# Kernel tuning notes

Measured on AMD Instinct MI355X. Metric: run time of the kernel, lower is better.

## Reference

```python
import jax, jax.numpy as jnp
import numpy as np

# Dims: N parameter samples, M patches, C tracked compartments (S is implicit),
# TIMESTEPS sequential SIR-metapopulation steps.
N, M, C, TIMESTEPS = 256, 128, 3, 200


def setup_inputs() -> dict:
    key = jax.random.key(0)
    k1, k2, k3, k4 = jax.random.split(key, 4)
    R = jax.random.uniform(k1, (N, M, M), jnp.float32)          # mobility matrix (row-normalized in reference)
    T = jax.random.uniform(k2, (N, C, C), jnp.float32) * 0.3    # compartment transition matrix (scaled so rho stays in [0,1])
    rho0 = jax.random.uniform(k3, (N, M, C), jnp.float32) * 0.01  # small initial infected fractions
    beta = jax.random.uniform(k4, (N, 1), jnp.float32) * 0.5    # per-sample infection rate (infect_params)
    return {"R": R, "T": T, "rho0": rho0, "beta": beta}


def _infect_prob(prev_rho, R, pop, neff, beta):
    # Contact infection ('beta_contact'):
    #   ninf[n,k] = sum_j pop[j] * prev_rho[n,j,0] * R[n,j,k]
    # This equals summing neff_compartments[..., 0] over the source-patch axis,
    # without materializing the (N, M, M, C) tensor the TF code builds.
    ninf = jnp.einsum('j,nj,njk->nk', pop, prev_rho[..., 0], R)
    return beta * ninf / neff  # (N, M)


def reference(R, T, rho0, beta):
    R = R / jnp.sum(R, axis=-1, keepdims=True)
    pop = jnp.ones((M,), R.dtype)  # default populations
    # neff = populations @ R; constant across timesteps, hoisted out of the loop
    neff = jnp.einsum('j,njk->nk', pop, R)  # (N, M)
    e0 = jnp.zeros((C,), R.dtype).at[0].set(1.0)  # new infections enter compartment 0

    def step(prev_rho, _):
        p = _infect_prob(prev_rho, R, pop, neff, beta)                    # (N, M)
        new_inf = (1.0 - prev_rho.sum(-1)) * jnp.einsum('njk,nk->nj', R, p)  # S * (R @ p)
        rho = jnp.einsum('njk,nkl->njl', prev_rho, T) + new_inf[:, :, None] * e0
        rho = jnp.clip(rho, 0.0, 1.0)
        return rho, prev_rho  # write prev_rho at step i, then advance (matches TF body)

    _, trajs = jax.lax.scan(step, rho0, None, length=TIMESTEPS)  # (T, N, M, C)
    trajs = trajs.astype(jnp.float32)
    # AddSusceptibleLayer: prepend S = 1 - sum(compartments), transpose to (N, T, M, C+1)
    S = 1.0 - trajs.sum(-1)
    out = jnp.concatenate([S[..., None], trajs], axis=-1)
    return jnp.transpose(out, (1, 0, 2, 3))
```

## Files before the change

### kernel.cpp

```cpp
#include <hip/hip_runtime.h>

namespace {

constexpr int NS = 256;
constexpr int MP = 128;
constexpr int TSTEPS = 200;
constexpr int BLK = 512;

typedef _Float16 half8 __attribute__((ext_vector_type(8)));
typedef float f32x4 __attribute__((ext_vector_type(4)));

__device__ __forceinline__ float4 ldg4(const float* p) {
  return *reinterpret_cast<const float4*>(p);
}
__device__ __forceinline__ float clamp01(float v) {
  return fminf(fmaxf(v, 0.0f), 1.0f);
}
__device__ __forceinline__ void step_barrier() {
  asm volatile("s_waitcnt lgkmcnt(0)" ::: "memory");
  __builtin_amdgcn_s_barrier();
  asm volatile("" ::: "memory");
}
__device__ __forceinline__ float dot2(unsigned a, unsigned b, float c) {
  float d;
  asm("v_dot2_f32_f16 %0, %1, %2, %3" : "=v"(d) : "v"(a), "v"(b), "v"(c));
  return d;
}
__device__ __forceinline__ unsigned pkrtz(float a, float b) {
  typedef __fp16 h2v __attribute__((ext_vector_type(2)));
  h2v r = __builtin_amdgcn_cvt_pkrtz(a, b);
  return __builtin_bit_cast(unsigned, r);
}
__device__ __forceinline__ float dpp_xor1(float x) {
  int yi = __builtin_amdgcn_update_dpp(0, __float_as_int(x), 0xB1, 0xF, 0xF, true);
  return __int_as_float(yi);
}
__device__ __forceinline__ int qidx16(int row, int ch) {
  return (row << 4) + (ch ^ ((row >> 3) & 7));
}
__device__ __forceinline__ half8 h8(uint4 v) {
  return __builtin_bit_cast(half8, v);
}

__global__ __launch_bounds__(BLK, 2)
void sir_meta_kernel(const float* __restrict__ Rg,
                     const float* __restrict__ Tg,
                     const float* __restrict__ rho0g,
                     const float* __restrict__ betag,
                     float* __restrict__ outg)
{
  __shared__ __align__(16) float rs[MP];
  __shared__ __align__(16) float sbin[MP];
  __shared__ __align__(16) float scr[BLK];
  __shared__ __align__(16) unsigned xh[2][64];
  __shared__ __align__(16) uint4 q16[MP * 16];
  __shared__ __align__(16) uint4 gh[MP * 16];

  const int tid = threadIdx.x;
  const int n = blockIdx.x;
  const float* __restrict__ Rn = Rg + (size_t)n * MP * MP;

  {
    const int wave = tid >> 6;
    const int lane = tid & 63;
    const int half = lane >> 5;
    const int l32 = lane & 31;
    for (int it = 0; it < 8; ++it) {
      const int row = wave * 16 + it * 2 + half;
      float4 v = ldg4(Rn + row * MP + l32 * 4);
      float s = (v.x + v.y) + (v.z + v.w);
      s += __shfl_xor(s, 1);
      s += __shfl_xor(s, 2);
      s += __shfl_xor(s, 4);
      s += __shfl_xor(s, 8);
      s += __shfl_xor(s, 16);
      if (l32 == 0) rs[row] = 1.0f / s;
    }
  }
  __syncthreads();

  {
    const int c = tid & 127;
    const int h = tid >> 7;
    float a = 0.0f;
    #pragma unroll 8
    for (int i = 0; i < 32; ++i) {
      const int ig = h * 32 + i;
      a = fmaf(Rn[ig * MP + c], rs[ig], a);
    }
    scr[tid] = a;
  }
  __syncthreads();
  if (tid < 128)
    sbin[tid] = sqrtf(betag[n] /
        (((scr[tid] + scr[tid + 128]) + (scr[tid + 256] + scr[tid + 384]))));
  __syncthreads();

  {
    #pragma unroll
    for (int u = 0; u < 4; ++u) {
      const int fi8 = u * BLK + tid;
      const int r = fi8 >> 4, c8 = fi8 & 15;
      float4 lo = ldg4(Rn + r * MP + c8 * 8);
      float4 hi = ldg4(Rn + r * MP + c8 * 8 + 4);
      float4 s0 = *reinterpret_cast<const float4*>(&sbin[c8 * 8]);
      float4 s1 = *reinterpret_cast<const float4*>(&sbin[c8 * 8 + 4]);
      uint4 w;
      w.x = pkrtz(lo.x * s0.x, lo.y * s0.y);
      w.y = pkrtz(lo.z * s0.z, lo.w * s0.w);
      w.z = pkrtz(hi.x * s1.x, hi.y * s1.y);
      w.w = pkrtz(hi.z * s1.z, hi.w * s1.w);
      q16[qidx16(r, c8)] = w;
    }
  }
  __syncthreads();

  {
    const int wv = tid >> 6;
    const int g4 = (tid >> 4) & 3;
    const int k4 = tid & 15;
    const int rb = wv * 16 + g4 * 4;
    const int cb = k4 * 8;
    float acc[4][8];
    #pragma unroll
    for (int r = 0; r < 4; ++r)
      #pragma unroll
      for (int c = 0; c < 8; ++c) acc[r][c] = 0.0f;
    #pragma unroll 4
    for (int ch = 0; ch < 16; ++ch) {
      uint4 qa[4], qb[8];
      #pragma unroll
      for (int r = 0; r < 4; ++r) qa[r] = q16[qidx16(rb + r, ch)];
      #pragma unroll
      for (int c = 0; c < 8; ++c) qb[c] = q16[qidx16(cb + c, ch)];
      #pragma unroll
      for (int r = 0; r < 4; ++r) {
        #pragma unroll
        for (int c = 0; c < 8; ++c) {
          float a = acc[r][c];
          a = dot2(qa[r].x, qb[c].x, a);
          a = dot2(qa[r].y, qb[c].y, a);
          a = dot2(qa[r].z, qb[c].z, a);
          a = dot2(qa[r].w, qb[c].w, a);
          acc[r][c] = a;
        }
      }
    }
    float rsc[8];
    #pragma unroll
    for (int c = 0; c < 8; ++c) rsc[c] = rs[cb + c];
    #pragma unroll
    for (int r = 0; r < 4; ++r) {
      const float rr = rs[rb + r];
      uint4 w;
      w.x = pkrtz(acc[r][0] * rr * rsc[0], acc[r][1] * rr * rsc[1]);
      w.y = pkrtz(acc[r][2] * rr * rsc[2], acc[r][3] * rr * rsc[3]);
      w.z = pkrtz(acc[r][4] * rr * rsc[4], acc[r][5] * rr * rsc[5]);
      w.w = pkrtz(acc[r][6] * rr * rsc[6], acc[r][7] * rr * rsc[7]);
      gh[(rb + r) * 16 + k4] = w;
    }
  }
  __syncthreads();

  const int w = tid >> 6;
  const int l = tid & 63;
  const int col = l & 15;
  const int kg = l >> 4;
  const int jrow = 16 * w + 4 * kg + col;
  const bool writer = (col < 4);

  uint4 af0 = gh[(16 * w + col) * 16 + 0 + kg];
  uint4 af1 = gh[(16 * w + col) * 16 + 4 + kg];
  uint4 af2 = gh[(16 * w + col) * 16 + 8 + kg];
  uint4 af3 = gh[(16 * w + col) * 16 + 12 + kg];

  const float* Tn = Tg + n * 9;
  const float T00 = Tn[0], T01 = Tn[1], T02 = Tn[2];
  const float T10 = Tn[3], T11 = Tn[4], T12 = Tn[5];
  const float T20 = Tn[6], T21 = Tn[7], T22 = Tn[8];

  float r0 = 0.f, r1 = 0.f, r2 = 0.f;
  if (writer) {
    const float* rp = rho0g + ((size_t)n * MP + jrow) * 3;
    r0 = rp[0]; r1 = rp[1]; r2 = rp[2];
  }
  if (tid < 64) {
    const float* xp = rho0g + ((size_t)n * MP + 2 * tid) * 3;
    xh[0][tid] = pkrtz(xp[0], xp[3]);
  }
  __syncthreads();

  float4* outp = reinterpret_cast<float4*>(outg) + (size_t)n * TSTEPS * MP + jrow;
  const bool xwriter = writer && ((col & 1) == 0);
  const int xslot = jrow >> 1;

  for (int s = 0; s < TSTEPS; ++s) {
    const uint4* xq4 = reinterpret_cast<const uint4*>(&xh[s & 1][0]);
    const uint4 b0 = xq4[kg];
    const uint4 b1 = xq4[4 + kg];
    const uint4 b2 = xq4[8 + kg];
    const uint4 b3 = xq4[12 + kg];

    const float S = 1.0f - ((r0 + r1) + r2);
    if (writer) *outp = make_float4(S, r0, r1, r2);
    outp += MP;

    f32x4 accA = {0.f, 0.f, 0.f, 0.f};
    f32x4 accB = {0.f, 0.f, 0.f, 0.f};
    accA = __builtin_amdgcn_mfma_f32_16x16x32_f16(h8(af0), h8(b0), accA, 0, 0, 0);
    accB = __builtin_amdgcn_mfma_f32_16x16x32_f16(h8(af1), h8(b1), accB, 0, 0, 0);
    accA = __builtin_amdgcn_mfma_f32_16x16x32_f16(h8(af2), h8(b2), accA, 0, 0, 0);
    accB = __builtin_amdgcn_mfma_f32_16x16x32_f16(h8(af3), h8(b3), accB, 0, 0, 0);

    const float tA0 = (col & 1) ? accA[1] : accA[0];
    const float tA1 = (col & 1) ? accA[3] : accA[2];
    const float tB0 = (col & 1) ? accB[1] : accB[0];
    const float tB1 = (col & 1) ? accB[3] : accB[2];
    const float y = ((col & 2) ? tA1 : tA0) + ((col & 2) ? tB1 : tB0);

    const float ni = S * y;
    const float n0 = clamp01(fmaf(r0, T00, fmaf(r1, T10, fmaf(r2, T20, ni))));
    const float n1 = clamp01(fmaf(r0, T01, fmaf(r1, T11, r2 * T21)));
    const float n2 = clamp01(fmaf(r0, T02, fmaf(r1, T12, r2 * T22)));

    const float nb = dpp_xor1(n0);
    if (xwriter) xh[(s & 1) ^ 1][xslot] = pkrtz(n0, nb);

    r0 = n0; r1 = n1; r2 = n2;

    step_barrier();
  }
}

}

extern "C" void kernel_launch(void* const* d_in, const int* in_sizes, int n_in,
                              void* d_out, int out_size, void* d_ws, size_t ws_size,
                              hipStream_t stream)
{
  const float* Rg    = (const float*)d_in[0];
  const float* Tg    = (const float*)d_in[1];
  const float* rho0g = (const float*)d_in[2];
  const float* betag = (const float*)d_in[3];
  float* outg = (float*)d_out;
  sir_meta_kernel<<<NS, BLK, 0, stream>>>(Rg, Tg, rho0g, betag, outg);
}
```

Measured before the change: 74.07 us.

## Replicate full mat-vec in every wave to drop per-step block barriers

Each wave now holds all 8 row-blocks of the fp16 G matrix in registers and computes the full 128-row mat-vec itself every step. The next step's B operand is exchanged with ds_bpermute inside the wave instead of through double-buffered LDS. This removes the block-wide barrier from every timestep. In exchange each wave issues 8x more MFMAs per step, raises register pressure from holding 32 uint4 fragments, and has each lane track two rows.

```diff
diff --git a/kernel.cpp b/kernel.cpp
--- a/kernel.cpp
+++ b/kernel.cpp
@@ -16,11 +16,6 @@
 __device__ __forceinline__ float clamp01(float v) {
   return fminf(fmaxf(v, 0.0f), 1.0f);
 }
-__device__ __forceinline__ void step_barrier() {
-  asm volatile("s_waitcnt lgkmcnt(0)" ::: "memory");
-  __builtin_amdgcn_s_barrier();
-  asm volatile("" ::: "memory");
-}
 __device__ __forceinline__ float dot2(unsigned a, unsigned b, float c) {
   float d;
   asm("v_dot2_f32_f16 %0, %1, %2, %3" : "=v"(d) : "v"(a), "v"(b), "v"(c));
@@ -31,9 +26,8 @@
   h2v r = __builtin_amdgcn_cvt_pkrtz(a, b);
   return __builtin_bit_cast(unsigned, r);
 }
-__device__ __forceinline__ float dpp_xor1(float x) {
-  int yi = __builtin_amdgcn_update_dpp(0, __float_as_int(x), 0xB1, 0xF, 0xF, true);
-  return __int_as_float(yi);
+__device__ __forceinline__ unsigned bperm(int addr, unsigned src) {
+  return (unsigned)__builtin_amdgcn_ds_bpermute(addr, (int)src);
 }
 __device__ __forceinline__ int qidx16(int row, int ch) {
   return (row << 4) + (ch ^ ((row >> 3) & 7));
@@ -52,7 +46,7 @@
   __shared__ __align__(16) float rs[MP];
   __shared__ __align__(16) float sbin[MP];
   __shared__ __align__(16) float scr[BLK];
-  __shared__ __align__(16) unsigned xh[2][64];
+  __shared__ __align__(16) unsigned xh[64];
   __shared__ __align__(16) uint4 q16[MP * 16];
   __shared__ __align__(16) uint4 gh[MP * 16];
 
@@ -160,75 +154,117 @@
       gh[(rb + r) * 16 + k4] = w;
     }
   }
+  if (tid < 64) {
+    const float* xp = rho0g + ((size_t)n * MP + 2 * tid) * 3;
+    xh[tid] = pkrtz(xp[0], xp[3]);
+  }
   __syncthreads();
 
   const int w = tid >> 6;
   const int l = tid & 63;
   const int col = l & 15;
   const int kg = l >> 4;
-  const int jrow = 16 * w + 4 * kg + col;
-  const bool writer = (col < 4);
-
-  uint4 af0 = gh[(16 * w + col) * 16 + 0 + kg];
-  uint4 af1 = gh[(16 * w + col) * 16 + 4 + kg];
-  uint4 af2 = gh[(16 * w + col) * 16 + 8 + kg];
-  uint4 af3 = gh[(16 * w + col) * 16 + 12 + kg];
+  const bool t1 = (col & 1) != 0;
+  const bool i0 = (col & 2) != 0;
+  const bool i1 = (col & 4) != 0;
+  const bool i2 = (col & 8) != 0;
+  const int Istar = col >> 1;
+  const int rowA = 16 * Istar + 4 * kg + 2 * (col & 1);
+
+  uint4 af[8][4];
+  #pragma unroll
+  for (int I = 0; I < 8; ++I)
+    #pragma unroll
+    for (int c = 0; c < 4; ++c)
+      af[I][c] = gh[(16 * I + col) * 16 + 4 * c + kg];
+
+  int baddr[4][4];
+  #pragma unroll
+  for (int c = 0; c < 4; ++c)
+    #pragma unroll
+    for (int j = 0; j < 4; ++j) {
+      const int m = 16 * c + 4 * kg + j;
+      baddr[c][j] = 4 * (2 * (m >> 3) + (m & 1) + 16 * ((m >> 1) & 3));
+    }
+
+  const uint4* xq4 = reinterpret_cast<const uint4*>(xh);
+  uint4 bf0 = xq4[kg];
+  uint4 bf1 = xq4[4 + kg];
+  uint4 bf2 = xq4[8 + kg];
+  uint4 bf3 = xq4[12 + kg];
 
   const float* Tn = Tg + n * 9;
   const float T00 = Tn[0], T01 = Tn[1], T02 = Tn[2];
   const float T10 = Tn[3], T11 = Tn[4], T12 = Tn[5];
   const float T20 = Tn[6], T21 = Tn[7], T22 = Tn[8];
 
-  float r0 = 0.f, r1 = 0.f, r2 = 0.f;
-  if (writer) {
-    const float* rp = rho0g + ((size_t)n * MP + jrow) * 3;
-    r0 = rp[0]; r1 = rp[1]; r2 = rp[2];
-  }
-  if (tid < 64) {
-    const float* xp = rho0g + ((size_t)n * MP + 2 * tid) * 3;
-    xh[0][tid] = pkrtz(xp[0], xp[3]);
-  }
-  __syncthreads();
-
-  float4* outp = reinterpret_cast<float4*>(outg) + (size_t)n * TSTEPS * MP + jrow;
-  const bool xwriter = writer && ((col & 1) == 0);
-  const int xslot = jrow >> 1;
+  const float* rp = rho0g + ((size_t)n * MP + rowA) * 3;
+  float a0 = rp[0], a1 = rp[1], a2 = rp[2];
+  float b0 = rp[3], b1 = rp[4], b2 = rp[5];
+
+  const bool storer = (Istar == w);
+  float4* outp = reinterpret_cast<float4*>(outg) + (size_t)n * TSTEPS * MP + rowA;
 
   for (int s = 0; s < TSTEPS; ++s) {
-    const uint4* xq4 = reinterpret_cast<const uint4*>(&xh[s & 1][0]);
-    const uint4 b0 = xq4[kg];
-    const uint4 b1 = xq4[4 + kg];
-    const uint4 b2 = xq4[8 + kg];
-    const uint4 b3 = xq4[12 + kg];
-
-    const float S = 1.0f - ((r0 + r1) + r2);
-    if (writer) *outp = make_float4(S, r0, r1, r2);
+    f32x4 acc[8];
+    #pragma unroll
+    for (int I = 0; I < 8; ++I) {
+      f32x4 a = {0.f, 0.f, 0.f, 0.f};
+      a = __builtin_amdgcn_mfma_f32_16x16x32_f16(h8(af[I][0]), h8(bf0), a, 0, 0, 0);
+      a = __builtin_amdgcn_mfma_f32_16x16x32_f16(h8(af[I][1]), h8(bf1), a, 0, 0, 0);
+      a = __builtin_amdgcn_mfma_f32_16x16x32_f16(h8(af[I][2]), h8(bf2), a, 0, 0, 0);
+      a = __builtin_amdgcn_mfma_f32_16x16x32_f16(h8(af[I][3]), h8(bf3), a, 0, 0, 0);
+      acc[I] = a;
+    }
+
+    const float SA = 1.0f - ((a0 + a1) + a2);
+    const float SB = 1.0f - ((b0 + b1) + b2);
+    if (storer) {
+      outp[0] = make_float4(SA, a0, a1, a2);
+      outp[1] = make_float4(SB, b0, b1, b2);
+    }
     outp += MP;
 
-    f32x4 accA = {0.f, 0.f, 0.f, 0.f};
-    f32x4 accB = {0.f, 0.f, 0.f, 0.f};
-    accA = __builtin_amdgcn_mfma_f32_16x16x32_f16(h8(af0), h8(b0), accA, 0, 0, 0);
-    accB = __builtin_amdgcn_mfma_f32_16x16x32_f16(h8(af1), h8(b1), accB, 0, 0, 0);
-    accA = __builtin_amdgcn_mfma_f32_16x16x32_f16(h8(af2), h8(b2), accA, 0, 0, 0);
-    accB = __builtin_amdgcn_mfma_f32_16x16x32_f16(h8(af3), h8(b3), accB, 0, 0, 0);
-
-    const float tA0 = (col & 1) ? accA[1] : accA[0];
-    const float tA1 = (col & 1) ? accA[3] : accA[2];
-    const float tB0 = (col & 1) ? accB[1] : accB[0];
-    const float tB1 = (col & 1) ? accB[3] : accB[2];
-    const float y = ((col & 2) ? tA1 : tA0) + ((col & 2) ? tB1 : tB0);
-
-    const float ni = S * y;
-    const float n0 = clamp01(fmaf(r0, T00, fmaf(r1, T10, fmaf(r2, T20, ni))));
-    const float n1 = clamp01(fmaf(r0, T01, fmaf(r1, T11, r2 * T21)));
-    const float n2 = clamp01(fmaf(r0, T02, fmaf(r1, T12, r2 * T22)));
-
-    const float nb = dpp_xor1(n0);
-    if (xwriter) xh[(s & 1) ^ 1][xslot] = pkrtz(n0, nb);
-
-    r0 = n0; r1 = n1; r2 = n2;
-
-    step_barrier();
+    float qA[8], qB[8];
+    #pragma unroll
+    for (int I = 0; I < 8; ++I) {
+      qA[I] = t1 ? acc[I][2] : acc[I][0];
+      qB[I] = t1 ? acc[I][3] : acc[I][1];
+    }
+    const float uA0 = i0 ? qA[1] : qA[0];
+    const float uA1 = i0 ? qA[3] : qA[2];
+    const float uA2 = i0 ? qA[5] : qA[4];
+    const float uA3 = i0 ? qA[7] : qA[6];
+    const float vA0 = i1 ? uA1 : uA0;
+    const float vA1 = i1 ? uA3 : uA2;
+    const float yA = i2 ? vA1 : vA0;
+    const float uB0 = i0 ? qB[1] : qB[0];
+    const float uB1 = i0 ? qB[3] : qB[2];
+    const float uB2 = i0 ? qB[5] : qB[4];
+    const float uB3 = i0 ? qB[7] : qB[6];
+    const float vB0 = i1 ? uB1 : uB0;
+    const float vB1 = i1 ? uB3 : uB2;
+    const float yB = i2 ? vB1 : vB0;
+
+    const float n0A = clamp01(fmaf(a0, T00, fmaf(a1, T10, fmaf(a2, T20, SA * yA))));
+    const float n0B = clamp01(fmaf(b0, T00, fmaf(b1, T10, fmaf(b2, T20, SB * yB))));
+    const unsigned xnew = pkrtz(n0A, n0B);
+
+    bf0 = make_uint4(bperm(baddr[0][0], xnew), bperm(baddr[0][1], xnew),
+                     bperm(baddr[0][2], xnew), bperm(baddr[0][3], xnew));
+    bf1 = make_uint4(bperm(baddr[1][0], xnew), bperm(baddr[1][1], xnew),
+                     bperm(baddr[1][2], xnew), bperm(baddr[1][3], xnew));
+    bf2 = make_uint4(bperm(baddr[2][0], xnew), bperm(baddr[2][1], xnew),
+                     bperm(baddr[2][2], xnew), bperm(baddr[2][3], xnew));
+    bf3 = make_uint4(bperm(baddr[3][0], xnew), bperm(baddr[3][1], xnew),
+                     bperm(baddr[3][2], xnew), bperm(baddr[3][3], xnew));
+
+    const float n1A = clamp01(fmaf(a0, T01, fmaf(a1, T11, a2 * T21)));
+    const float n2A = clamp01(fmaf(a0, T02, fmaf(a1, T12, a2 * T22)));
+    const float n1B = clamp01(fmaf(b0, T01, fmaf(b1, T11, b2 * T21)));
+    const float n2B = clamp01(fmaf(b0, T02, fmaf(b1, T12, b2 * T22)));
+    a0 = n0A; a1 = n1A; a2 = n2A;
+    b0 = n0B; b1 = n1B; b2 = n2B;
   }
 }
 
```

Result: slower. 181.6 us (+145.2%).

## Compute R·diag(beta/neff)·Rᵀ precompute with MFMA instead of dot2 loops

Applied to the files above, without the earlier changes.

The one-time G = R diag(beta/neff) Rᵀ matrix product in the prologue now runs on 16x16x32 f16 MFMA instructions instead of scalar v_dot2 loops. The beta/neff scaling is applied to one operand as packed f16 multiplies rather than as a sqrt split across both sides. The rho0 staging into xh is moved before the barrier, which removes one __syncthreads. The prologue cost shrinks, but rounding changes a little because beta/neff is now quantised to f16 directly on one side.

```diff
diff --git a/kernel.cpp b/kernel.cpp
--- a/kernel.cpp
+++ b/kernel.cpp
@@ -8,6 +8,7 @@
 constexpr int BLK = 512;
 
 typedef _Float16 half8 __attribute__((ext_vector_type(8)));
+typedef __fp16 h8v __attribute__((ext_vector_type(8)));
 typedef float f32x4 __attribute__((ext_vector_type(4)));
 
 __device__ __forceinline__ float4 ldg4(const float* p) {
@@ -21,15 +22,16 @@
   __builtin_amdgcn_s_barrier();
   asm volatile("" ::: "memory");
 }
-__device__ __forceinline__ float dot2(unsigned a, unsigned b, float c) {
-  float d;
-  asm("v_dot2_f32_f16 %0, %1, %2, %3" : "=v"(d) : "v"(a), "v"(b), "v"(c));
-  return d;
-}
 __device__ __forceinline__ unsigned pkrtz(float a, float b) {
   typedef __fp16 h2v __attribute__((ext_vector_type(2)));
   h2v r = __builtin_amdgcn_cvt_pkrtz(a, b);
   return __builtin_bit_cast(unsigned, r);
+}
+__device__ __forceinline__ uint4 pkmul4(uint4 a, uint4 b) {
+  h8v x = __builtin_bit_cast(h8v, a);
+  h8v y = __builtin_bit_cast(h8v, b);
+  h8v z = x * y;
+  return __builtin_bit_cast(uint4, z);
 }
 __device__ __forceinline__ float dpp_xor1(float x) {
   int yi = __builtin_amdgcn_update_dpp(0, __float_as_int(x), 0xB1, 0xF, 0xF, true);
@@ -50,7 +52,8 @@
                      float* __restrict__ outg)
 {
   __shared__ __align__(16) float rs[MP];
-  __shared__ __align__(16) float sbin[MP];
+  __shared__ __align__(16) float bnv[MP];
+  __shared__ __align__(16) unsigned binv16[64];
   __shared__ __align__(16) float scr[BLK];
   __shared__ __align__(16) unsigned xh[2][64];
   __shared__ __align__(16) uint4 q16[MP * 16];
@@ -92,8 +95,8 @@
   }
   __syncthreads();
   if (tid < 128)
-    sbin[tid] = sqrtf(betag[n] /
-        (((scr[tid] + scr[tid + 128]) + (scr[tid + 256] + scr[tid + 384]))));
+    bnv[tid] = betag[n] /
+        (((scr[tid] + scr[tid + 128]) + (scr[tid + 256] + scr[tid + 384])));
   __syncthreads();
 
   {
@@ -103,62 +106,53 @@
       const int r = fi8 >> 4, c8 = fi8 & 15;
       float4 lo = ldg4(Rn + r * MP + c8 * 8);
       float4 hi = ldg4(Rn + r * MP + c8 * 8 + 4);
-      float4 s0 = *reinterpret_cast<const float4*>(&sbin[c8 * 8]);
-      float4 s1 = *reinterpret_cast<const float4*>(&sbin[c8 * 8 + 4]);
       uint4 w;
-      w.x = pkrtz(lo.x * s0.x, lo.y * s0.y);
-      w.y = pkrtz(lo.z * s0.z, lo.w * s0.w);
-      w.z = pkrtz(hi.x * s1.x, hi.y * s1.y);
-      w.w = pkrtz(hi.z * s1.z, hi.w * s1.w);
+      w.x = pkrtz(lo.x, lo.y);
+      w.y = pkrtz(lo.z, lo.w);
+      w.z = pkrtz(hi.x, hi.y);
+      w.w = pkrtz(hi.z, hi.w);
       q16[qidx16(r, c8)] = w;
     }
-  }
-  __syncthreads();
-
-  {
-    const int wv = tid >> 6;
-    const int g4 = (tid >> 4) & 3;
-    const int k4 = tid & 15;
-    const int rb = wv * 16 + g4 * 4;
-    const int cb = k4 * 8;
-    float acc[4][8];
+    if (tid < 64) binv16[tid] = pkrtz(bnv[2 * tid], bnv[2 * tid + 1]);
+  }
+  __syncthreads();
+
+  {
+    const int J = tid >> 6;
+    const int l = tid & 63;
+    const int col = l & 15;
+    const int kg = l >> 4;
+    const uint4* bnv4 = reinterpret_cast<const uint4*>(binv16);
+    uint4 bfj[4];
     #pragma unroll
-    for (int r = 0; r < 4; ++r)
-      #pragma unroll
-      for (int c = 0; c < 8; ++c) acc[r][c] = 0.0f;
-    #pragma unroll 4
-    for (int ch = 0; ch < 16; ++ch) {
-      uint4 qa[4], qb[8];
-      #pragma unroll
-      for (int r = 0; r < 4; ++r) qa[r] = q16[qidx16(rb + r, ch)];
-      #pragma unroll
-      for (int c = 0; c < 8; ++c) qb[c] = q16[qidx16(cb + c, ch)];
+    for (int c = 0; c < 4; ++c)
+      bfj[c] = pkmul4(q16[qidx16(16 * J + col, 4 * c + kg)], bnv4[4 * c + kg]);
+    const float rscol = rs[16 * J + col];
+    unsigned* ghu = reinterpret_cast<unsigned*>(gh);
+    #pragma unroll
+    for (int I = 0; I < 8; ++I) {
+      const uint4 af0 = q16[qidx16(16 * I + col, 0 + kg)];
+      const uint4 af1 = q16[qidx16(16 * I + col, 4 + kg)];
+      const uint4 af2 = q16[qidx16(16 * I + col, 8 + kg)];
+      const uint4 af3 = q16[qidx16(16 * I + col, 12 + kg)];
+      f32x4 a = {0.f, 0.f, 0.f, 0.f};
+      a = __builtin_amdgcn_mfma_f32_16x16x32_f16(h8(af0), h8(bfj[0]), a, 0, 0, 0);
+      a = __builtin_amdgcn_mfma_f32_16x16x32_f16(h8(af1), h8(bfj[1]), a, 0, 0, 0);
+      a = __builtin_amdgcn_mfma_f32_16x16x32_f16(h8(af2), h8(bfj[2]), a, 0, 0, 0);
+      a = __builtin_amdgcn_mfma_f32_16x16x32_f16(h8(af3), h8(bfj[3]), a, 0, 0, 0);
       #pragma unroll
       for (int r = 0; r < 4; ++r) {
-        #pragma unroll
-        for (int c = 0; c < 8; ++c) {
-          float a = acc[r][c];
-          a = dot2(qa[r].x, qb[c].x, a);
-          a = dot2(qa[r].y, qb[c].y, a);
-          a = dot2(qa[r].z, qb[c].z, a);
-          a = dot2(qa[r].w, qb[c].w, a);
-          acc[r][c] = a;
-        }
+        const int ROW = 16 * I + 4 * kg + r;
+        const float val = a[r] * rs[ROW] * rscol;
+        const float nb = dpp_xor1(val);
+        if ((col & 1) == 0)
+          ghu[ROW * 64 + 8 * J + (col >> 1)] = pkrtz(val, nb);
       }
     }
-    float rsc[8];
-    #pragma unroll
-    for (int c = 0; c < 8; ++c) rsc[c] = rs[cb + c];
-    #pragma unroll
-    for (int r = 0; r < 4; ++r) {
-      const float rr = rs[rb + r];
-      uint4 w;
-      w.x = pkrtz(acc[r][0] * rr * rsc[0], acc[r][1] * rr * rsc[1]);
-      w.y = pkrtz(acc[r][2] * rr * rsc[2], acc[r][3] * rr * rsc[3]);
-      w.z = pkrtz(acc[r][4] * rr * rsc[4], acc[r][5] * rr * rsc[5]);
-      w.w = pkrtz(acc[r][6] * rr * rsc[6], acc[r][7] * rr * rsc[7]);
-      gh[(rb + r) * 16 + k4] = w;
-    }
+  }
+  if (tid < 64) {
+    const float* xp = rho0g + ((size_t)n * MP + 2 * tid) * 3;
+    xh[0][tid] = pkrtz(xp[0], xp[3]);
   }
   __syncthreads();
 
@@ -184,11 +178,6 @@
     const float* rp = rho0g + ((size_t)n * MP + jrow) * 3;
     r0 = rp[0]; r1 = rp[1]; r2 = rp[2];
   }
-  if (tid < 64) {
-    const float* xp = rho0g + ((size_t)n * MP + 2 * tid) * 3;
-    xh[0][tid] = pkrtz(xp[0], xp[3]);
-  }
-  __syncthreads();
 
   float4* outp = reinterpret_cast<float4*>(outg) + (size_t)n * TSTEPS * MP + jrow;
   const bool xwriter = writer && ((col & 1) == 0);
```

New measurement: 70.38 us. -5.0%, faster.
